# Kernel tuning notes

Hardware: AMD Instinct MI355X
Metric: run time of the kernel (lower is better)

## Reference

```python
import jax, jax.numpy as jnp
import numpy as np

DIM = 256
HEADS = 8
DIM_HEAD = 32
HIDDEN = HEADS * DIM_HEAD  # 256
SCALE = DIM_HEAD ** -0.5


def setup_inputs() -> dict:
    key = jax.random.key(0)
    k1, k2, k3, k4 = jax.random.split(key, 4)
    x = jax.random.normal(k1, (1, DIM, 16, 16, 16), dtype=jnp.float32)
    # 1x1x1 Conv3d weights are plain channel-mixing matrices
    w_qkv = jax.random.normal(k2, (3 * HIDDEN, DIM), dtype=jnp.float32) * (DIM ** -0.5)
    w_out = jax.random.normal(k3, (DIM, HIDDEN), dtype=jnp.float32) * (HIDDEN ** -0.5)
    b_out = jax.random.normal(k4, (DIM,), dtype=jnp.float32) * 0.01
    return {"x": x, "w_qkv": w_qkv, "w_out": w_out, "b_out": b_out}


def reference(x, w_qkv, w_out, b_out):
    b, c, X, Y, Z = x.shape
    n = X * Y * Z
    xf = x.reshape(b, c, n)                                   # b c n
    qkv = jnp.einsum('oc,bcn->bon', w_qkv, xf)                # b 3H n
    q, k, v = jnp.split(qkv, 3, axis=1)                       # each b (h c) n
    def heads(t):
        return t.reshape(b, HEADS, DIM_HEAD, n)               # b h c n
    q, k, v = heads(q) * SCALE, heads(k), heads(v)
    sim = jnp.einsum('bhci,bhcj->bhij', q, k)                 # b h n n
    attn = jax.nn.softmax(sim, axis=-1)
    out = jnp.einsum('bhij,bhcj->bhci', attn, v)              # b h c n
    out = out.reshape(b, HIDDEN, n)                           # b (h c) n
    out = jnp.einsum('oc,bcn->bon', w_out, out) + b_out[None, :, None]
    return out.reshape(b, DIM, X, Y, Z)
```

## Files before the change

### kernel.cpp

```cpp
#include <hip/hip_runtime.h>
#include <hip/hip_bf16.h>
#include <cstdint>


typedef __bf16 bf16x8 __attribute__((ext_vector_type(8)));
typedef float f32x4 __attribute__((ext_vector_type(4)));
typedef float f32x16 __attribute__((ext_vector_type(16)));
typedef unsigned int u32;
typedef unsigned short u16;
typedef u32 u32x4v __attribute__((ext_vector_type(4)));
typedef u32 u32x2v __attribute__((ext_vector_type(2)));

#define MFMA16(a, b, c) __builtin_amdgcn_mfma_f32_16x16x32_bf16(a, b, c, 0, 0, 0)
#define MFMA32(a, b, c) __builtin_amdgcn_mfma_f32_32x32x16_bf16(a, b, c, 0, 0, 0)

#if __has_builtin(__builtin_amdgcn_exp2f)
#define EXP2(x) __builtin_amdgcn_exp2f(x)
#else
#define EXP2(x) exp2f(x)
#endif

__device__ __forceinline__ u16 f2bf(float f) {
  __bf16 b = (__bf16)f;
  return __builtin_bit_cast(u16, b);
}
__device__ __forceinline__ u32 pk2(float a, float b) {
  return (u32)f2bf(a) | ((u32)f2bf(b) << 16);
}
__device__ __forceinline__ bf16x8 ldfrag(const u16* p) {
  return __builtin_bit_cast(bf16x8, *(const u32x4v*)p);
}
__device__ __forceinline__ void gload_lds16(const void* g, void* l) {
  __builtin_amdgcn_global_load_lds((const __attribute__((address_space(1))) u32*)g,
                                   (__attribute__((address_space(3))) u32*)l, 16, 0, 0);
}
__device__ __forceinline__ void plswap(u32& a, u32& b) {
  asm("v_permlane32_swap_b32 %0, %1" : "+v"(a), "+v"(b));
}
__device__ __forceinline__ f32x16 zero16() {
  f32x16 z;
#pragma unroll
  for (int i = 0; i < 16; ++i) z[i] = 0.0f;
  return z;
}

#if __has_builtin(__builtin_amdgcn_fdot2_f32_bf16)
typedef __bf16 bf16x2 __attribute__((ext_vector_type(2)));
__device__ __forceinline__ float dot2one(u32 pk, float acc) {
  const u32 one2 = 0x3F803F80u;
  return __builtin_amdgcn_fdot2_f32_bf16(__builtin_bit_cast(bf16x2, pk),
                                         __builtin_bit_cast(bf16x2, one2), acc, false);
}
#define LSUM_STEP(LSUM, P, PK)                               \
  {                                                          \
    _Pragma("unroll") for (int m_ = 0; m_ < 8; ++m_) LSUM =  \
        dot2one(PK[m_], LSUM);                               \
  }
#else
#define LSUM_STEP(LSUM, P, PK)                               \
  {                                                          \
    float t0_ = (P[0] + P[1]) + (P[2] + P[3]);               \
    float t1_ = (P[4] + P[5]) + (P[6] + P[7]);               \
    float t2_ = (P[8] + P[9]) + (P[10] + P[11]);             \
    float t3_ = (P[12] + P[13]) + (P[14] + P[15]);           \
    LSUM += (t0_ + t1_) + (t2_ + t3_);                       \
  }
#endif

__global__ __launch_bounds__(256) void qkv_gemm(const float* __restrict__ x,
                                                const float* __restrict__ wq,
                                                u16* __restrict__ qT, u16* __restrict__ kT,
                                                u16* __restrict__ vv) {
  __shared__ __align__(16) u16 Al[64 * 64];
  __shared__ __align__(16) u16 Bl[128 * 64];
  const int t = threadIdx.x;
  const int lane = t & 63, w = t >> 6;
  const int wm = w & 1, wn = w >> 1;
  const int o0 = blockIdx.y * 64, n0 = blockIdx.x * 128;
  const int lr = lane & 15, lg = lane >> 4;
  const float sc = (o0 < 256) ? 0.2550349f : 1.0f;
  f32x4 acc[2][4];
#pragma unroll
  for (int i = 0; i < 2; ++i)
#pragma unroll
    for (int j = 0; j < 4; ++j)
#pragma unroll
      for (int r = 0; r < 4; ++r) acc[i][j][r] = 0.0f;

  for (int kc = 0; kc < 256; kc += 64) {
#pragma unroll
    for (int r = 0; r < 4; ++r) {
      int idx = r * 256 + t;
      int o = idx >> 4, c4 = (idx & 15) << 2;
      float4 v4 = *(const float4*)(wq + (size_t)(o0 + o) * 256 + kc + c4);
      u32x2v pkd;
      pkd.x = pk2(v4.x * sc, v4.y * sc);
      pkd.y = pk2(v4.z * sc, v4.w * sc);
      *(u32x2v*)&Al[o * 64 + (c4 ^ ((o & 7) << 3))] = pkd;
    }
#pragma unroll
    for (int r = 0; r < 8; ++r) {
      int idx = r * 256 + t;
      int n = idx & 127, cg = idx >> 7;
      int c4 = cg << 2;
      const float* xb = x + (size_t)(kc + c4) * 4096 + n0 + n;
      float a0 = xb[0], a1 = xb[4096], a2 = xb[8192], a3 = xb[12288];
      u32x2v pkd;
      pkd.x = pk2(a0, a1);
      pkd.y = pk2(a2, a3);
      *(u32x2v*)&Bl[n * 64 + (c4 ^ ((n & 7) << 3))] = pkd;
    }
    __syncthreads();
#pragma unroll
    for (int kk = 0; kk < 2; ++kk) {
      bf16x8 af[2], bf_[4];
#pragma unroll
      for (int mi = 0; mi < 2; ++mi) {
        int row = wm * 32 + mi * 16 + lr;
        af[mi] = ldfrag(&Al[row * 64 + ((kk * 32 + lg * 8) ^ ((row & 7) << 3))]);
      }
#pragma unroll
      for (int ni = 0; ni < 4; ++ni) {
        int row = wn * 64 + ni * 16 + lr;
        bf_[ni] = ldfrag(&Bl[row * 64 + ((kk * 32 + lg * 8) ^ ((row & 7) << 3))]);
      }
#pragma unroll
      for (int mi = 0; mi < 2; ++mi)
#pragma unroll
        for (int ni = 0; ni < 4; ++ni) acc[mi][ni] = MFMA16(af[mi], bf_[ni], acc[mi][ni]);
    }
    __syncthreads();
  }
#pragma unroll
  for (int mi = 0; mi < 2; ++mi) {
#pragma unroll
    for (int ni = 0; ni < 4; ++ni) {
      int obase = o0 + wm * 32 + mi * 16 + lg * 4;
      int n = n0 + wn * 64 + ni * 16 + lr;
      int part = obase >> 8;
      int oin = obase & 255;
      int h = oin >> 5, c0 = oin & 31;
      if (part == 0) {
        u32x2v pv;
        pv.x = pk2(acc[mi][ni][0], acc[mi][ni][1]);
        pv.y = pk2(acc[mi][ni][2], acc[mi][ni][3]);
        *(u32x2v*)(qT + ((size_t)h * 4096 + n) * 32 + c0) = pv;
      } else if (part == 1) {
        u32x2v pv;
        pv.x = pk2(acc[mi][ni][0], acc[mi][ni][1]);
        pv.y = pk2(acc[mi][ni][2], acc[mi][ni][3]);
        *(u32x2v*)(kT + ((size_t)h * 4096 + n) * 32 + c0) = pv;
      } else {
#pragma unroll
        for (int r = 0; r < 4; ++r)
          vv[((size_t)h * 32 + c0 + r) * 4096 + n] = f2bf(acc[mi][ni][r]);
      }
    }
  }
}


#define LOAD_TILE(KV0, K0, K1, V0, V1)                            \
  do {                                                            \
    const u16* kp_ = kTh + (size_t)((KV0) + l31) * 32 + lh * 8;   \
    K0 = ldfrag(kp_);                                             \
    K1 = ldfrag(kp_ + 16);                                        \
    const u16* vp_ = vh + (size_t)l31 * 4096 + (KV0) + lh * 8;    \
    V0 = ldfrag(vp_);                                             \
    V1 = ldfrag(vp_ + 16);                                        \
  } while (0)

#define COMPUTE_IT(QF0, QF1, OACC, LSUM, K0, K1, V0, V1)                      \
  do {                                                                        \
    f32x16 sT_ = zero16();                                                    \
    sT_ = MFMA32(K0, QF0, sT_);                  \
    sT_ = MFMA32(K1, QF1, sT_);                                               \
    float p_[16];                                                             \
    _Pragma("unroll") for (int r_ = 0; r_ < 16; ++r_) p_[r_] = EXP2(sT_[r_]); \
    u32 pkv_[8];                                                              \
    _Pragma("unroll") for (int m_ = 0; m_ < 8; ++m_) pkv_[m_] =               \
        pk2(p_[2 * m_], p_[2 * m_ + 1]);                                      \
    LSUM_STEP(LSUM, p_, pkv_)                                                 \
    u32 ax_ = pkv_[0], bx_ = pkv_[2];                                         \
    plswap(ax_, bx_);                                                         \
    u32 ay_ = pkv_[1], by_ = pkv_[3];                                         \
    plswap(ay_, by_);                                                         \
    u32 cx_ = pkv_[4], dx_ = pkv_[6];                                         \
    plswap(cx_, dx_);                                                         \
    u32 cy_ = pkv_[5], dy_ = pkv_[7];                                         \
    plswap(cy_, dy_);                                                         \
    u32x4v f1_, f2_;                                                          \
    f1_.x = ax_; f1_.y = ay_; f1_.z = bx_; f1_.w = by_;                       \
    f2_.x = cx_; f2_.y = cy_; f2_.z = dx_; f2_.w = dy_;                       \
    OACC = MFMA32(V0, __builtin_bit_cast(bf16x8, f1_), OACC);                 \
    OACC = MFMA32(V1, __builtin_bit_cast(bf16x8, f2_), OACC);                 \
  } while (0)

__global__ __launch_bounds__(512, 4) void attn_fused(const u16* __restrict__ qT,
                                                     const u16* __restrict__ kT,
                                                     const u16* __restrict__ vv,
                                                     u16* __restrict__ aout) {
  __shared__ float pbuf[8 * 32 * 66];
  __shared__ float lbuf[8 * 64];
  const int tid = threadIdx.x;
  const int lane = tid & 63, s = tid >> 6;
  const int qb = blockIdx.x, h = blockIdx.y;
  const int l31 = lane & 31, lh = lane >> 5;
  const u16* qTh = qT + (size_t)h * (4096 * 32);
  const u16* kTh = kT + (size_t)h * (4096 * 32);
  const u16* vh = vv + (size_t)h * (32 * 4096);

  const int i0 = qb * 64 + l31;
  bf16x8 qf00 = ldfrag(qTh + (size_t)i0 * 32 + lh * 8);
  bf16x8 qf01 = ldfrag(qTh + (size_t)i0 * 32 + 16 + lh * 8);
  bf16x8 qf10 = ldfrag(qTh + (size_t)(i0 + 32) * 32 + lh * 8);
  bf16x8 qf11 = ldfrag(qTh + (size_t)(i0 + 32) * 32 + 16 + lh * 8);

  f32x16 oacc0 = zero16(), oacc1 = zero16();
  float lsum0 = 0.0f, lsum1 = 0.0f;
  const int kvbase = s * 512;

  bf16x8 ka0, ka1, va0, va1, kb0, kb1, vb0, vb1;
  LOAD_TILE(kvbase, ka0, ka1, va0, va1);
  for (int tt = 0; tt < 16; tt += 2) {
    LOAD_TILE(kvbase + (tt + 1) * 32, kb0, kb1, vb0, vb1);
    COMPUTE_IT(qf00, qf01, oacc0, lsum0, ka0, ka1, va0, va1);
    COMPUTE_IT(qf10, qf11, oacc1, lsum1, ka0, ka1, va0, va1);
    if (tt + 2 < 16) LOAD_TILE(kvbase + (tt + 2) * 32, ka0, ka1, va0, va1);
    COMPUTE_IT(qf00, qf01, oacc0, lsum0, kb0, kb1, vb0, vb1);
    COMPUTE_IT(qf10, qf11, oacc1, lsum1, kb0, kb1, vb0, vb1);
  }

  float ls0 = lsum0 + __shfl_xor(lsum0, 32, 64);
  float ls1 = lsum1 + __shfl_xor(lsum1, 32, 64);
#pragma unroll
  for (int r = 0; r < 16; ++r) {
    int c = (r & 3) + 8 * (r >> 2) + 4 * lh;
    pbuf[(s * 32 + c) * 66 + l31] = oacc0[r];
    pbuf[(s * 32 + c) * 66 + 32 + l31] = oacc1[r];
  }
  lbuf[s * 64 + l31] = ls0;
  lbuf[s * 64 + 32 + l31] = ls1;
  __syncthreads();

  {
    int i = tid >> 3, c0 = (tid & 7) << 2;
    float lt = 0.0f;
#pragma unroll
    for (int ss = 0; ss < 8; ++ss) lt += lbuf[ss * 64 + i];
    float inv = 1.0f / lt;
    float a[4];
#pragma unroll
    for (int cc = 0; cc < 4; ++cc) a[cc] = 0.0f;
#pragma unroll
    for (int ss = 0; ss < 8; ++ss)
#pragma unroll
      for (int cc = 0; cc < 4; ++cc) a[cc] += pbuf[(ss * 32 + c0 + cc) * 66 + i];
    u32x2v ov;
    ov.x = pk2(a[0] * inv, a[1] * inv);
    ov.y = pk2(a[2] * inv, a[3] * inv);
    *(u32x2v*)(aout + (size_t)(qb * 64 + i) * 256 + h * 32 + c0) = ov;
  }
}

__global__ __launch_bounds__(256) void out_proj(const float* __restrict__ wo,
                                                const float* __restrict__ bo,
                                                const u16* __restrict__ aout,
                                                float* __restrict__ out) {
  __shared__ __align__(16) u16 Al[64 * 64];
  __shared__ __align__(16) u16 Bl[64 * 64];
  const int t = threadIdx.x;
  const int lane = t & 63, w = t >> 6;
  const int n0 = blockIdx.x * 64, d0 = blockIdx.y * 64;
  const int lr = lane & 15, lg = lane >> 4;
  f32x4 acc[4];
#pragma unroll
  for (int ni = 0; ni < 4; ++ni)
#pragma unroll
    for (int r = 0; r < 4; ++r) acc[ni][r] = 0.0f;

  for (int kc = 0; kc < 256; kc += 64) {
#pragma unroll
    for (int r = 0; r < 4; ++r) {
      int idx = r * 256 + t;
      int d = idx >> 4, c4 = (idx & 15) << 2;
      float4 v4 = *(const float4*)(wo + (size_t)(d0 + d) * 256 + kc + c4);
      u32x2v pkd;
      pkd.x = pk2(v4.x, v4.y);
      pkd.y = pk2(v4.z, v4.w);
      *(u32x2v*)&Al[d * 64 + (c4 ^ ((d & 7) << 3))] = pkd;
    }
#pragma unroll
    for (int q = 0; q < 2; ++q) {
      int nrow = q * 32 + w * 8 + (lane >> 3);
      int cb = ((lane & 7) << 4) ^ ((nrow & 7) << 4);
      gload_lds16((const char*)aout + (size_t)(n0 + nrow) * 512 + kc * 2 + cb,
                  (void*)&Bl[(q * 32 + w * 8) * 64]);
    }
    __syncthreads();
#pragma unroll
    for (int kk = 0; kk < 2; ++kk) {
      int arow = w * 16 + lr;
      bf16x8 af = ldfrag(&Al[arow * 64 + ((kk * 32 + lg * 8) ^ ((arow & 7) << 3))]);
#pragma unroll
      for (int ni = 0; ni < 4; ++ni) {
        int brow = ni * 16 + lr;
        bf16x8 bfr = ldfrag(&Bl[brow * 64 + ((kk * 32 + lg * 8) ^ ((brow & 7) << 3))]);
        acc[ni] = MFMA16(af, bfr, acc[ni]);
      }
    }
    __syncthreads();
  }
#pragma unroll
  for (int ni = 0; ni < 4; ++ni) {
    int n = n0 + ni * 16 + lr;
#pragma unroll
    for (int r = 0; r < 4; ++r) {
      int d = d0 + w * 16 + lg * 4 + r;
      out[(size_t)d * 4096 + n] = acc[ni][r] + bo[d];
    }
  }
}

extern "C" void kernel_launch(void* const* d_in, const int* in_sizes, int n_in,
                              void* d_out, int out_size, void* d_ws, size_t ws_size,
                              hipStream_t stream) {
  (void)in_sizes; (void)n_in; (void)out_size; (void)ws_size;
  const float* x = (const float*)d_in[0];
  const float* wqkv = (const float*)d_in[1];
  const float* wout = (const float*)d_in[2];
  const float* bout = (const float*)d_in[3];
  float* out = (float*)d_out;
  u16* qT = (u16*)d_ws;
  u16* kT = qT + 8 * 4096 * 32;
  u16* vv = kT + 8 * 4096 * 32;
  u16* aout = vv + 8 * 32 * 4096;

  qkv_gemm<<<dim3(32, 12), 256, 0, stream>>>(x, wqkv, qT, kT, vv);
  attn_fused<<<dim3(64, 8), 512, 0, stream>>>(qT, kT, vv, aout);
  out_proj<<<dim3(64, 4), 256, 0, stream>>>(wout, bout, aout, out);
}
```

Baseline: 55.79 us.

## Add prep kernel converting inputs to bf16 and use direct global-to-LDS loads

Adds a prep kernel that transposes x to bf16 [n][c] and converts the QKV and output weights to bf16 (Q pre-scaled). Both GEMMs can then fill their swizzled LDS tiles with direct global-to-LDS 16-byte loads instead of strided fp32 loads and conversions. The QKV GEMM tile along n is halved so it launches twice as many blocks. MFMA regions in attention are also wrapped in s_setprio. The cost is an extra kernel launch plus a round trip through workspace memory.

```diff
diff --git a/kernel.cpp b/kernel.cpp
--- a/kernel.cpp
+++ b/kernel.cpp
@@ -67,76 +67,119 @@
   }
 #endif
 
-__global__ __launch_bounds__(256) void qkv_gemm(const float* __restrict__ x,
-                                                const float* __restrict__ wq,
+__global__ __launch_bounds__(256) void prep(const float* __restrict__ x,
+                                            const float* __restrict__ wq,
+                                            const float* __restrict__ wo,
+                                            u16* __restrict__ xT, u16* __restrict__ wqb,
+                                            u16* __restrict__ wob) {
+  const int b = blockIdx.x;
+  const int t = threadIdx.x;
+  if (b < 256) {
+    __shared__ u16 tile[64][72];
+    const int n0 = (b & 63) * 64, c0 = (b >> 6) * 64;
+#pragma unroll
+    for (int r = 0; r < 4; ++r) {
+      int c = r * 16 + (t >> 4);
+      int n4 = (t & 15) << 2;
+      float4 v = *(const float4*)(x + (size_t)(c0 + c) * 4096 + n0 + n4);
+      tile[n4 + 0][c] = f2bf(v.x);
+      tile[n4 + 1][c] = f2bf(v.y);
+      tile[n4 + 2][c] = f2bf(v.z);
+      tile[n4 + 3][c] = f2bf(v.w);
+    }
+    __syncthreads();
+#pragma unroll
+    for (int r2 = 0; r2 < 2; ++r2) {
+      int n = r2 * 32 + (t >> 3);
+      int c8 = (t & 7) << 3;
+      u32x4v o;
+#pragma unroll
+      for (int j = 0; j < 4; ++j)
+        o[j] = (u32)tile[n][c8 + 2 * j] | ((u32)tile[n][c8 + 2 * j + 1] << 16);
+      *(u32x4v*)(xT + (size_t)(n0 + n) * 256 + c0 + c8) = o;
+    }
+  } else if (b < 304) {
+    int base = (b - 256) * 4096;
+#pragma unroll
+    for (int r = 0; r < 4; ++r) {
+      int i = base + r * 1024 + t * 4;
+      float4 v = *(const float4*)(wq + i);
+      float sc = (i < 65536) ? 0.2550349f : 1.0f;
+      u32x2v pkd;
+      pkd.x = pk2(v.x * sc, v.y * sc);
+      pkd.y = pk2(v.z * sc, v.w * sc);
+      *(u32x2v*)(wqb + i) = pkd;
+    }
+  } else {
+    int base = (b - 304) * 4096;
+#pragma unroll
+    for (int r = 0; r < 4; ++r) {
+      int i = base + r * 1024 + t * 4;
+      float4 v = *(const float4*)(wo + i);
+      u32x2v pkd;
+      pkd.x = pk2(v.x, v.y);
+      pkd.y = pk2(v.z, v.w);
+      *(u32x2v*)(wob + i) = pkd;
+    }
+  }
+}
+
+__global__ __launch_bounds__(256) void qkv_gemm(const u16* __restrict__ xT,
+                                                const u16* __restrict__ wqb,
                                                 u16* __restrict__ qT, u16* __restrict__ kT,
                                                 u16* __restrict__ vv) {
   __shared__ __align__(16) u16 Al[64 * 64];
-  __shared__ __align__(16) u16 Bl[128 * 64];
+  __shared__ __align__(16) u16 Bl[64 * 64];
   const int t = threadIdx.x;
   const int lane = t & 63, w = t >> 6;
   const int wm = w & 1, wn = w >> 1;
-  const int o0 = blockIdx.y * 64, n0 = blockIdx.x * 128;
+  const int o0 = blockIdx.y * 64, n0 = blockIdx.x * 64;
   const int lr = lane & 15, lg = lane >> 4;
-  const float sc = (o0 < 256) ? 0.2550349f : 1.0f;
-  f32x4 acc[2][4];
+  const int srow = lane >> 3, sslot = lane & 7;
+  f32x4 acc[2][2];
 #pragma unroll
   for (int i = 0; i < 2; ++i)
 #pragma unroll
-    for (int j = 0; j < 4; ++j)
+    for (int j = 0; j < 2; ++j)
 #pragma unroll
       for (int r = 0; r < 4; ++r) acc[i][j][r] = 0.0f;
 
   for (int kc = 0; kc < 256; kc += 64) {
 #pragma unroll
-    for (int r = 0; r < 4; ++r) {
-      int idx = r * 256 + t;
-      int o = idx >> 4, c4 = (idx & 15) << 2;
-      float4 v4 = *(const float4*)(wq + (size_t)(o0 + o) * 256 + kc + c4);
-      u32x2v pkd;
-      pkd.x = pk2(v4.x * sc, v4.y * sc);
-      pkd.y = pk2(v4.z * sc, v4.w * sc);
-      *(u32x2v*)&Al[o * 64 + (c4 ^ ((o & 7) << 3))] = pkd;
-    }
-#pragma unroll
-    for (int r = 0; r < 8; ++r) {
-      int idx = r * 256 + t;
-      int n = idx & 127, cg = idx >> 7;
-      int c4 = cg << 2;
-      const float* xb = x + (size_t)(kc + c4) * 4096 + n0 + n;
-      float a0 = xb[0], a1 = xb[4096], a2 = xb[8192], a3 = xb[12288];
-      u32x2v pkd;
-      pkd.x = pk2(a0, a1);
-      pkd.y = pk2(a2, a3);
-      *(u32x2v*)&Bl[n * 64 + (c4 ^ ((n & 7) << 3))] = pkd;
+    for (int rnd = 0; rnd < 2; ++rnd) {
+      int row = rnd * 32 + w * 8 + srow;
+      gload_lds16(wqb + (size_t)(o0 + row) * 256 + kc + ((sslot ^ (row & 7)) << 3),
+                  (void*)(Al + rnd * 2048 + w * 512));
+      gload_lds16(xT + (size_t)(n0 + row) * 256 + kc + ((sslot ^ (row & 7)) << 3),
+                  (void*)(Bl + rnd * 2048 + w * 512));
     }
     __syncthreads();
 #pragma unroll
     for (int kk = 0; kk < 2; ++kk) {
-      bf16x8 af[2], bf_[4];
+      bf16x8 af[2], bf_[2];
 #pragma unroll
       for (int mi = 0; mi < 2; ++mi) {
         int row = wm * 32 + mi * 16 + lr;
         af[mi] = ldfrag(&Al[row * 64 + ((kk * 32 + lg * 8) ^ ((row & 7) << 3))]);
       }
 #pragma unroll
-      for (int ni = 0; ni < 4; ++ni) {
-        int row = wn * 64 + ni * 16 + lr;
+      for (int ni = 0; ni < 2; ++ni) {
+        int row = wn * 32 + ni * 16 + lr;
         bf_[ni] = ldfrag(&Bl[row * 64 + ((kk * 32 + lg * 8) ^ ((row & 7) << 3))]);
       }
 #pragma unroll
       for (int mi = 0; mi < 2; ++mi)
 #pragma unroll
-        for (int ni = 0; ni < 4; ++ni) acc[mi][ni] = MFMA16(af[mi], bf_[ni], acc[mi][ni]);
+        for (int ni = 0; ni < 2; ++ni) acc[mi][ni] = MFMA16(af[mi], bf_[ni], acc[mi][ni]);
     }
     __syncthreads();
   }
 #pragma unroll
   for (int mi = 0; mi < 2; ++mi) {
 #pragma unroll
-    for (int ni = 0; ni < 4; ++ni) {
+    for (int ni = 0; ni < 2; ++ni) {
       int obase = o0 + wm * 32 + mi * 16 + lg * 4;
-      int n = n0 + wn * 64 + ni * 16 + lr;
+      int n = n0 + wn * 32 + ni * 16 + lr;
       int part = obase >> 8;
       int oin = obase & 255;
       int h = oin >> 5, c0 = oin & 31;
@@ -173,8 +216,10 @@
 #define COMPUTE_IT(QF0, QF1, OACC, LSUM, K0, K1, V0, V1)                      \
   do {                                                                        \
     f32x16 sT_ = zero16();                                                    \
+    __builtin_amdgcn_s_setprio(1);                                            \
     sT_ = MFMA32(K0, QF0, sT_);                  \
     sT_ = MFMA32(K1, QF1, sT_);                                               \
+    __builtin_amdgcn_s_setprio(0);                                            \
     float p_[16];                                                             \
     _Pragma("unroll") for (int r_ = 0; r_ < 16; ++r_) p_[r_] = EXP2(sT_[r_]); \
     u32 pkv_[8];                                                              \
@@ -192,8 +237,10 @@
     u32x4v f1_, f2_;                                                          \
     f1_.x = ax_; f1_.y = ay_; f1_.z = bx_; f1_.w = by_;                       \
     f2_.x = cx_; f2_.y = cy_; f2_.z = dx_; f2_.w = dy_;                       \
+    __builtin_amdgcn_s_setprio(1);                                            \
     OACC = MFMA32(V0, __builtin_bit_cast(bf16x8, f1_), OACC);                 \
     OACC = MFMA32(V1, __builtin_bit_cast(bf16x8, f2_), OACC);                 \
+    __builtin_amdgcn_s_setprio(0);                                            \
   } while (0)
 
 __global__ __launch_bounds__(512, 4) void attn_fused(const u16* __restrict__ qT,
@@ -263,7 +310,7 @@
   }
 }
 
-__global__ __launch_bounds__(256) void out_proj(const float* __restrict__ wo,
+__global__ __launch_bounds__(256) void out_proj(const u16* __restrict__ wob,
                                                 const float* __restrict__ bo,
                                                 const u16* __restrict__ aout,
                                                 float* __restrict__ out) {
@@ -273,6 +320,7 @@
   const int lane = t & 63, w = t >> 6;
   const int n0 = blockIdx.x * 64, d0 = blockIdx.y * 64;
   const int lr = lane & 15, lg = lane >> 4;
+  const int srow = lane >> 3, sslot = lane & 7;
   f32x4 acc[4];
 #pragma unroll
   for (int ni = 0; ni < 4; ++ni)
@@ -281,21 +329,12 @@
 
   for (int kc = 0; kc < 256; kc += 64) {
 #pragma unroll
-    for (int r = 0; r < 4; ++r) {
-      int idx = r * 256 + t;
-      int d = idx >> 4, c4 = (idx & 15) << 2;
-      float4 v4 = *(const float4*)(wo + (size_t)(d0 + d) * 256 + kc + c4);
-      u32x2v pkd;
-      pkd.x = pk2(v4.x, v4.y);
-      pkd.y = pk2(v4.z, v4.w);
-      *(u32x2v*)&Al[d * 64 + (c4 ^ ((d & 7) << 3))] = pkd;
-    }
-#pragma unroll
-    for (int q = 0; q < 2; ++q) {
-      int nrow = q * 32 + w * 8 + (lane >> 3);
-      int cb = ((lane & 7) << 4) ^ ((nrow & 7) << 4);
-      gload_lds16((const char*)aout + (size_t)(n0 + nrow) * 512 + kc * 2 + cb,
-                  (void*)&Bl[(q * 32 + w * 8) * 64]);
+    for (int rnd = 0; rnd < 2; ++rnd) {
+      int row = rnd * 32 + w * 8 + srow;
+      gload_lds16(wob + (size_t)(d0 + row) * 256 + kc + ((sslot ^ (row & 7)) << 3),
+                  (void*)(Al + rnd * 2048 + w * 512));
+      gload_lds16(aout + (size_t)(n0 + row) * 256 + kc + ((sslot ^ (row & 7)) << 3),
+                  (void*)(Bl + rnd * 2048 + w * 512));
     }
     __syncthreads();
 #pragma unroll
@@ -335,8 +374,12 @@
   u16* kT = qT + 8 * 4096 * 32;
   u16* vv = kT + 8 * 4096 * 32;
   u16* aout = vv + 8 * 32 * 4096;
-
-  qkv_gemm<<<dim3(32, 12), 256, 0, stream>>>(x, wqkv, qT, kT, vv);
+  u16* xT = aout + 4096 * 256;
+  u16* wqb = xT + 4096 * 256;
+  u16* wob = wqb + 768 * 256;
+
+  prep<<<320, 256, 0, stream>>>(x, wqkv, wout, xT, wqb, wob);
+  qkv_gemm<<<dim3(64, 12), 256, 0, stream>>>(xT, wqb, qT, kT, vv);
   attn_fused<<<dim3(64, 8), 512, 0, stream>>>(qT, kT, vv, aout);
-  out_proj<<<dim3(64, 4), 256, 0, stream>>>(wout, bout, aout, out);
-}
+  out_proj<<<dim3(64, 4), 256, 0, stream>>>(wob, bout, aout, out);
+}
```

Measured after the change: 52.68 us. 5.6% less time.
